# Optimization experiments

Measured on AMD Instinct MI355X. Metric: run time of the kernel, lower is better.

The kernel has to match this reference:

```python
import jax, jax.numpy as jnp
import numpy as np

NUM_HEADS = 16


def setup_inputs() -> dict:
    key = jax.random.key(0)
    ks = jax.random.split(key, 4)
    B, S, D = 2, 2048, 1024
    scale = 1.0 / np.sqrt(D)
    x = jax.random.normal(ks[0], (B, S, D), dtype=jnp.float32)
    Wq = jax.random.normal(ks[1], (D, D), dtype=jnp.float32) * scale
    Wk = jax.random.normal(ks[2], (D, D), dtype=jnp.float32) * scale
    Wv = jax.random.normal(ks[3], (D, D), dtype=jnp.float32) * scale
    bq = jnp.zeros((D,), dtype=jnp.float32)
    bk = jnp.zeros((D,), dtype=jnp.float32)
    bv = jnp.zeros((D,), dtype=jnp.float32)
    return {"x": x, "Wq": Wq, "bq": bq, "Wk": Wk, "bk": bk, "Wv": Wv, "bv": bv}


def _split_heads(t, H):
    B, S, D = t.shape
    return t.reshape(B, S, H, D // H).transpose(0, 2, 1, 3)  # (B,H,S,depth)


def reference(x, Wq, bq, Wk, bk, Wv, bv):
    H = NUM_HEADS
    B, S, D = x.shape
    depth = D // H
    q = _split_heads(x @ Wq + bq, H)
    k = _split_heads(x @ Wk + bk, H)
    v = _split_heads(x @ Wv + bv, H)
    # causal mask: strictly-upper-triangular ones, added as finfo.min * mask
    mask = 1.0 - jnp.tril(jnp.ones((S, S), dtype=jnp.float32))
    scores = jnp.einsum("bhqd,bhkd->bhqk", q, k) / jnp.sqrt(jnp.float32(depth))
    scores = scores + jnp.float32(np.finfo(np.float32).min) * mask
    probs = jax.nn.softmax(scores, axis=-1)
    att = jnp.einsum("bhqk,bhkd->bhqd", probs, v)
    return att.transpose(0, 2, 1, 3).reshape(B, S, D)
```

## Files before the change

### kernel.cpp

```cpp
#include <hip/hip_runtime.h>
#include <hip/hip_bf16.h>

#define B_ 2
#define S_ 2048
#define D_ 1024
#define H_ 16
#define DH 64
#define M_ (B_*S_)
#define NT_ (S_/64)

using bf16x8 = __attribute__((ext_vector_type(8))) __bf16;
using f32x4  = __attribute__((ext_vector_type(4))) float;

__device__ __forceinline__ int swz(int row) { return ((row ^ (row >> 3)) & 7) << 3; }

__device__ __forceinline__ void glds16(const __bf16* g, __bf16* l) {
#if __has_builtin(__builtin_amdgcn_global_load_lds)
  __builtin_amdgcn_global_load_lds(
      (const __attribute__((address_space(1))) unsigned int*)g,
      (__attribute__((address_space(3))) unsigned int*)l, 16, 0, 0);
#else
  *(bf16x8*)l = *(const bf16x8*)g;
#endif
}

__global__ __launch_bounds__(256) void conv_x(const float* __restrict__ x,
                                              __bf16* __restrict__ xb) {
  int idx = blockIdx.x * 256 + threadIdx.x;
  int m = idx >> 7, k = (idx & 127) * 8;
  float4 a = *(const float4*)&x[(size_t)m * D_ + k];
  float4 b = *(const float4*)&x[(size_t)m * D_ + k + 4];
  bf16x8 o;
  o[0]=(__bf16)a.x; o[1]=(__bf16)a.y; o[2]=(__bf16)a.z; o[3]=(__bf16)a.w;
  o[4]=(__bf16)b.x; o[5]=(__bf16)b.y; o[6]=(__bf16)b.z; o[7]=(__bf16)b.w;
  *(bf16x8*)&xb[(size_t)m * D_ + (k & ~63) + ((k & 63) ^ swz(m))] = o;
}

__global__ __launch_bounds__(256) void conv_w(const float* __restrict__ Wq,
                                              const float* __restrict__ Wk,
                                              const float* __restrict__ Wv,
                                              __bf16* __restrict__ wt) {
  int z = blockIdx.z;
  const float* __restrict__ W = (z == 0) ? Wq : (z == 1) ? Wk : Wv;
  __bf16* __restrict__ Wt = wt + (size_t)z * D_ * D_;
  __shared__ __bf16 Lt[64 * 66];
  int tid = threadIdx.x;
  int k0 = blockIdx.x * 64, n0 = blockIdx.y * 64;
  #pragma unroll
  for (int i = 0; i < 4; ++i) {
    int f4 = i * 256 + tid;
    int r = f4 >> 4, c4 = (f4 & 15) * 4;
    float4 v = *(const float4*)&W[(size_t)(k0 + r) * D_ + n0 + c4];
    Lt[(c4 + 0) * 66 + r] = (__bf16)v.x;
    Lt[(c4 + 1) * 66 + r] = (__bf16)v.y;
    Lt[(c4 + 2) * 66 + r] = (__bf16)v.z;
    Lt[(c4 + 3) * 66 + r] = (__bf16)v.w;
  }
  __syncthreads();
  #pragma unroll
  for (int i = 0; i < 2; ++i) {
    int idx = i * 256 + tid;
    int n = idx >> 3, kc = (idx & 7) * 8;
    int nf = n0 + n;
    bf16x8 o;
    #pragma unroll
    for (int j = 0; j < 8; ++j) o[j] = Lt[n * 66 + kc + j];
    *(bf16x8*)&Wt[(size_t)nf * D_ + k0 + (kc ^ swz(nf))] = o;
  }
}

#define BM 256
#define BN 256
#define BK 64
#define NKT (D_/BK)

__global__ __launch_bounds__(512) void qkv_gemm(
    const __bf16* __restrict__ xb, const __bf16* __restrict__ wt,
    const float* __restrict__ bq, const float* __restrict__ bk,
    const float* __restrict__ bv, __bf16* __restrict__ qkv) {
  int z = blockIdx.z;
  const __bf16* __restrict__ Wt = wt + (size_t)z * D_ * D_;
  const float* __restrict__ bias = (z == 0) ? bq : (z == 1) ? bk : bv;
  __bf16* __restrict__ out = qkv + (size_t)z * M_ * D_;
  const float scale = (z == 0) ? 0.125f : 1.0f;

  __shared__ __bf16 Al[2][BM * BK];
  __shared__ __bf16 Bl[2][BM * BK];

  int tid = threadIdx.x, lane = tid & 63, w = tid >> 6;
  int m0 = blockIdx.y * BM, n0 = blockIdx.x * BN;
  int wr = (w >> 2) * 128;
  int wc = (w & 3) * 64;

  f32x4 acc[8][4] = {};

#define STAGE(buf, kt)                                                        \
  {                                                                           \
    int k0 = (kt) * BK;                                                       \
    _Pragma("unroll")                                                         \
    for (int r = 0; r < 4; ++r) {                                             \
      int e = (r * 512 + tid) * 8;                                            \
      int row = e >> 6, col = e & 63;                                         \
      glds16(&xb[(size_t)(m0 + row) * D_ + k0 + col], &Al[buf][e]);           \
      glds16(&Wt[(size_t)(n0 + row) * D_ + k0 + col], &Bl[buf][e]);           \
    }                                                                         \
  }

  STAGE(0, 0);
  __syncthreads();

  int cur = 0;
  for (int kt = 0; kt < NKT; ++kt) {
    if (kt + 1 < NKT) STAGE(cur ^ 1, kt + 1);
    #pragma unroll
    for (int kk = 0; kk < 2; ++kk) {
      bf16x8 af[8], bfr[4];
      #pragma unroll
      for (int mi = 0; mi < 8; ++mi) {
        int row = wr + mi * 16 + (lane & 15);
        af[mi] = *(const bf16x8*)&Al[cur][row * 64 +
                 ((kk * 32 + (lane >> 4) * 8) ^ swz(row))];
      }
      #pragma unroll
      for (int ni = 0; ni < 4; ++ni) {
        int col = wc + ni * 16 + (lane & 15);
        bfr[ni] = *(const bf16x8*)&Bl[cur][col * 64 +
                  ((kk * 32 + (lane >> 4) * 8) ^ swz(col))];
      }
      #pragma unroll
      for (int mi = 0; mi < 8; ++mi)
        #pragma unroll
        for (int ni = 0; ni < 4; ++ni)
          acc[mi][ni] = __builtin_amdgcn_mfma_f32_16x16x32_bf16(
              af[mi], bfr[ni], acc[mi][ni], 0, 0, 0);
    }
    __syncthreads();
    cur ^= 1;
  }
#undef STAGE

  #pragma unroll
  for (int mi = 0; mi < 8; ++mi) {
    #pragma unroll
    for (int ni = 0; ni < 4; ++ni) {
      int col = n0 + wc + ni * 16 + (lane & 15);
      int h = col >> 6, dh = col & 63;
      float bv_ = bias[col];
      #pragma unroll
      for (int r = 0; r < 4; ++r) {
        int row = m0 + wr + mi * 16 + (lane >> 4) * 4 + r;
        int b = row >> 11, s = row & 2047;
        out[((size_t)(b * H_ + h) * S_ + s) * DH + dh] =
            (__bf16)((acc[mi][ni][r] + bv_) * scale);
      }
    }
  }
}

__global__ __launch_bounds__(256) void vtrans(const __bf16* __restrict__ v,
                                              __bf16* __restrict__ vt) {
  __shared__ __bf16 Lt[64 * 64];
  int tid = threadIdx.x;
  int s0 = blockIdx.x * 64;
  int h = blockIdx.y, b = blockIdx.z;
  const __bf16* __restrict__ src = v + ((size_t)(b * H_ + h)) * S_ * DH;
  __bf16* __restrict__ dst = vt + ((size_t)(b * H_ + h)) * DH * S_;
  #pragma unroll
  for (int i = 0; i < 2; ++i) {
    int e = (i * 256 + tid) * 8;
    int s = e >> 6, d0 = e & 63;
    bf16x8 r = *(const bf16x8*)&src[(size_t)(s0 + s) * DH + d0];
    #pragma unroll
    for (int j = 0; j < 8; ++j) {
      int d = d0 + j;
      Lt[d * 64 + (s ^ swz(d))] = r[j];
    }
  }
  __syncthreads();
  #pragma unroll
  for (int i = 0; i < 2; ++i) {
    int e = (i * 256 + tid) * 8;
    int d = e >> 6, sc = e & 63;
    bf16x8 o = *(const bf16x8*)&Lt[d * 64 + (sc ^ swz(d))];
    *(bf16x8*)&dst[(size_t)d * S_ + s0 + sc] = o;
  }
}

__device__ __forceinline__ void attn_tile_sw(
    const bf16x8* aq, f32x4* accO, float& m_reg, float& l_reg,
    const __bf16* __restrict__ Kl, const __bf16* __restrict__ Vt,
    __bf16* __restrict__ Plw, int lane, int kv0, int qbase, bool diag) {
  const int g = lane >> 4;
  const int ql = lane & 15;
  f32x4 sfT[4];
  __builtin_amdgcn_s_setprio(1);
  #pragma unroll
  for (int f = 0; f < 4; ++f) {
    f32x4 zz = {};
    int row = f * 16 + ql;
    int sr = swz(row);
    #pragma unroll
    for (int kk = 0; kk < 2; ++kk) {
      bf16x8 ka = *(const bf16x8*)&Kl[row * 64 + ((kk * 32 + g * 8) ^ sr)];
      zz = __builtin_amdgcn_mfma_f32_16x16x32_bf16(ka, aq[kk], zz, 0, 0, 0);
    }
    sfT[f] = zz;
  }
  __builtin_amdgcn_s_setprio(0);

  if (diag) {
    int qg = qbase + ql;
    #pragma unroll
    for (int f = 0; f < 4; ++f)
      #pragma unroll
      for (int r = 0; r < 4; ++r)
        if (kv0 + f * 16 + g * 4 + r > qg) sfT[f][r] = -1e30f;
  }

  float mx = sfT[0][0];
  #pragma unroll
  for (int f = 0; f < 4; ++f)
    #pragma unroll
    for (int r = 0; r < 4; ++r) mx = fmaxf(mx, sfT[f][r]);
  mx = fmaxf(mx, __shfl_xor(mx, 16, 64));
  mx = fmaxf(mx, __shfl_xor(mx, 32, 64));
  float mnew = fmaxf(m_reg, mx);
  float alpha = __expf(m_reg - mnew);
  m_reg = mnew;
  float rs = 0.f;
  #pragma unroll
  for (int f = 0; f < 4; ++f)
    #pragma unroll
    for (int r = 0; r < 4; ++r) {
      float p = __expf(sfT[f][r] - mnew);
      sfT[f][r] = p;
      rs += p;
    }
  rs += __shfl_xor(rs, 16, 64);
  rs += __shfl_xor(rs, 32, 64);
  l_reg = l_reg * alpha + rs;

  const int key = (ql & 7) << 3;
  #pragma unroll
  for (int f = 0; f < 4; ++f)
    #pragma unroll
    for (int r = 0; r < 4; ++r)
      Plw[ql * 64 + ((f * 16 + g * 4 + r) ^ key)] = (__bf16)sfT[f][r];

  float ab[4];
  #pragma unroll
  for (int r = 0; r < 4; ++r) ab[r] = __shfl(alpha, g * 4 + r, 16);
  #pragma unroll
  for (int f = 0; f < 4; ++f)
    #pragma unroll
    for (int r = 0; r < 4; ++r) accO[f][r] *= ab[r];

  __builtin_amdgcn_s_setprio(1);
  #pragma unroll
  for (int kk = 0; kk < 2; ++kk) {
    bf16x8 pa = *(const bf16x8*)&Plw[ql * 64 + ((kk * 32 + g * 8) ^ key)];
    #pragma unroll
    for (int f = 0; f < 4; ++f) {
      int vrow = f * 16 + ql;
      bf16x8 vb = *(const bf16x8*)&Vt[vrow * 64 + ((kk * 32 + g * 8) ^ swz(vrow))];
      accO[f] = __builtin_amdgcn_mfma_f32_16x16x32_bf16(pa, vb, accO[f], 0, 0, 0);
    }
  }
  __builtin_amdgcn_s_setprio(0);
}

__device__ __forceinline__ void attn_out_sw(
    const f32x4* accO, float l_reg, float* __restrict__ out,
    int b, int h, int qbase, int lane) {
  float lr[4];
  #pragma unroll
  for (int r = 0; r < 4; ++r) lr[r] = __shfl(l_reg, (lane >> 4) * 4 + r, 16);
  #pragma unroll
  for (int f = 0; f < 4; ++f) {
    int dh = f * 16 + (lane & 15);
    #pragma unroll
    for (int r = 0; r < 4; ++r) {
      int qg = qbase + (lane >> 4) * 4 + r;
      out[((size_t)(b * S_ + qg)) * D_ + h * DH + dh] = accO[f][r] / lr[r];
    }
  }
}

__global__ __launch_bounds__(256) void attn(
    const __bf16* __restrict__ Q, const __bf16* __restrict__ K,
    const __bf16* __restrict__ VT, float* __restrict__ out) {
  __shared__ __bf16 Kl[64 * 64];
  __shared__ __bf16 Vt[64 * 64];
  __shared__ __bf16 Pl[4][16 * 64];

  int tid = threadIdx.x, lane = tid & 63, w = tid >> 6;
  int bx = blockIdx.x, h = blockIdx.y, b = blockIdx.z;
  int qA0 = bx * 64, qB0 = (NT_ - 1 - bx) * 64;
  size_t base = ((size_t)(b * H_ + h)) * S_ * DH;
  const __bf16* __restrict__ Qg = Q + base;
  const __bf16* __restrict__ Kg = K + base;
  const __bf16* __restrict__ VTg = VT + base;

  bf16x8 aqA[2], aqB[2];
  int qra = qA0 + w * 16 + (lane & 15), qrb = qB0 + w * 16 + (lane & 15);
  #pragma unroll
  for (int kk = 0; kk < 2; ++kk) {
    aqA[kk] = *(const bf16x8*)&Qg[(size_t)qra * DH + kk * 32 + (lane >> 4) * 8];
    aqB[kk] = *(const bf16x8*)&Qg[(size_t)qrb * DH + kk * 32 + (lane >> 4) * 8];
  }

  f32x4 accA[4] = {}, accB[4] = {};
  float mA = -1e30f, lA = 0.f, mB = -1e30f, lB = 0.f;

  const int ktA = bx, ktB = NT_ - 1 - bx;

  bf16x8 kreg[2], vreg[2];
  #pragma unroll
  for (int i = 0; i < 2; ++i) {
    int e = (i * 256 + tid) * 8;
    kreg[i] = *(const bf16x8*)&Kg[(size_t)(e >> 6) * DH + (e & 63)];
    vreg[i] = *(const bf16x8*)&VTg[(size_t)(e >> 6) * S_ + (e & 63)];
  }

  for (int kt = 0; kt <= ktB; ++kt) {
    int kv0 = kt * 64;
    #pragma unroll
    for (int i = 0; i < 2; ++i) {
      int e = (i * 256 + tid) * 8;
      int rrow = e >> 6, cc = e & 63;
      *(bf16x8*)&Kl[rrow * 64 + (cc ^ swz(rrow))] = kreg[i];
      *(bf16x8*)&Vt[rrow * 64 + (cc ^ swz(rrow))] = vreg[i];
    }
    __syncthreads();

    if (kt < ktB) {
      int kvn = kv0 + 64;
      #pragma unroll
      for (int i = 0; i < 2; ++i) {
        int e = (i * 256 + tid) * 8;
        kreg[i] = *(const bf16x8*)&Kg[(size_t)(kvn + (e >> 6)) * DH + (e & 63)];
        vreg[i] = *(const bf16x8*)&VTg[(size_t)(e >> 6) * S_ + kvn + (e & 63)];
      }
    }

    attn_tile_sw(aqB, accB, mB, lB, Kl, Vt, Pl[w], lane, kv0, qB0 + w * 16,
                 kt == ktB);
    if (kt <= ktA)
      attn_tile_sw(aqA, accA, mA, lA, Kl, Vt, Pl[w], lane, kv0, qA0 + w * 16,
                   kt == ktA);
    __syncthreads();
  }

  attn_out_sw(accA, lA, out, b, h, qA0 + w * 16, lane);
  attn_out_sw(accB, lB, out, b, h, qB0 + w * 16, lane);
}

extern "C" void kernel_launch(void* const* d_in, const int* in_sizes, int n_in,
                              void* d_out, int out_size, void* d_ws, size_t ws_size,
                              hipStream_t stream) {
  const float* x  = (const float*)d_in[0];
  const float* Wq = (const float*)d_in[1];
  const float* bq = (const float*)d_in[2];
  const float* Wk = (const float*)d_in[3];
  const float* bk = (const float*)d_in[4];
  const float* Wv = (const float*)d_in[5];
  const float* bv = (const float*)d_in[6];
  float* out = (float*)d_out;

  __bf16* xb  = (__bf16*)d_ws;
  __bf16* wt  = xb + (size_t)M_ * D_;
  __bf16* qkv = wt + (size_t)3 * D_ * D_;
  __bf16* wsq = qkv;
  __bf16* wsk = qkv + (size_t)M_ * D_;
  __bf16* wsv = qkv + (size_t)2 * M_ * D_;
  __bf16* vtg = xb;

  conv_x<<<(M_ * (D_ / 8)) / 256, 256, 0, stream>>>(x, xb);
  conv_w<<<dim3(D_ / 64, D_ / 64, 3), 256, 0, stream>>>(Wq, Wk, Wv, wt);
  qkv_gemm<<<dim3(D_ / BN, M_ / BM, 3), 512, 0, stream>>>(xb, wt, bq, bk, bv, qkv);
  vtrans<<<dim3(S_ / 64, H_, B_), 256, 0, stream>>>(wsv, vtg);
  attn<<<dim3(NT_ / 2, H_, B_), 256, 0, stream>>>(wsq, wsk, vtg, out);
}
```

Measured before the change: 189.6 us.

## Shrink QKV GEMM tiles and streamline softmax with exp2, lazy rescale, packed bf16

The QKV GEMM moves from 256x256 tiles with 512 threads to 128x128 tiles with 256 threads. That raises the block count from 192 to 768, which should fill the CUs better at some cost in data reuse. The attention softmax folds log2(e) into the Q scale so it can use exp2f, and it skips rescaling the accumulator and running sum unless the max rises past a threshold, for which it relies on a warp-wide vote. P is converted to bf16 two values at a time with v_cvt_pk_bf16_f32 in inline asm, and the max reduction is restructured as a tree.

```diff
diff --git a/kernel.cpp b/kernel.cpp
--- a/kernel.cpp
+++ b/kernel.cpp
@@ -69,12 +69,10 @@
   }
 }
 
-#define BM 256
-#define BN 256
 #define BK 64
 #define NKT (D_/BK)
 
-__global__ __launch_bounds__(512) void qkv_gemm(
+__global__ __launch_bounds__(256) void qkv_gemm(
     const __bf16* __restrict__ xb, const __bf16* __restrict__ wt,
     const float* __restrict__ bq, const float* __restrict__ bk,
     const float* __restrict__ bv, __bf16* __restrict__ qkv) {
@@ -82,24 +80,23 @@
   const __bf16* __restrict__ Wt = wt + (size_t)z * D_ * D_;
   const float* __restrict__ bias = (z == 0) ? bq : (z == 1) ? bk : bv;
   __bf16* __restrict__ out = qkv + (size_t)z * M_ * D_;
-  const float scale = (z == 0) ? 0.125f : 1.0f;
-
-  __shared__ __bf16 Al[2][BM * BK];
-  __shared__ __bf16 Bl[2][BM * BK];
+  const float scale = (z == 0) ? 0.18033688f : 1.0f;
+
+  __shared__ __bf16 Al[2][128 * 64];
+  __shared__ __bf16 Bl[2][128 * 64];
 
   int tid = threadIdx.x, lane = tid & 63, w = tid >> 6;
-  int m0 = blockIdx.y * BM, n0 = blockIdx.x * BN;
-  int wr = (w >> 2) * 128;
-  int wc = (w & 3) * 64;
-
-  f32x4 acc[8][4] = {};
+  int m0 = blockIdx.y * 128, n0 = blockIdx.x * 128;
+  int wr = (w >> 1) * 64, wc = (w & 1) * 64;
+
+  f32x4 acc[4][4] = {};
 
 #define STAGE(buf, kt)                                                        \
   {                                                                           \
     int k0 = (kt) * BK;                                                       \
     _Pragma("unroll")                                                         \
     for (int r = 0; r < 4; ++r) {                                             \
-      int e = (r * 512 + tid) * 8;                                            \
+      int e = (r * 256 + tid) * 8;                                            \
       int row = e >> 6, col = e & 63;                                         \
       glds16(&xb[(size_t)(m0 + row) * D_ + k0 + col], &Al[buf][e]);           \
       glds16(&Wt[(size_t)(n0 + row) * D_ + k0 + col], &Bl[buf][e]);           \
@@ -114,9 +111,9 @@
     if (kt + 1 < NKT) STAGE(cur ^ 1, kt + 1);
     #pragma unroll
     for (int kk = 0; kk < 2; ++kk) {
-      bf16x8 af[8], bfr[4];
-      #pragma unroll
-      for (int mi = 0; mi < 8; ++mi) {
+      bf16x8 af[4], bfr[4];
+      #pragma unroll
+      for (int mi = 0; mi < 4; ++mi) {
         int row = wr + mi * 16 + (lane & 15);
         af[mi] = *(const bf16x8*)&Al[cur][row * 64 +
                  ((kk * 32 + (lane >> 4) * 8) ^ swz(row))];
@@ -128,7 +125,7 @@
                   ((kk * 32 + (lane >> 4) * 8) ^ swz(col))];
       }
       #pragma unroll
-      for (int mi = 0; mi < 8; ++mi)
+      for (int mi = 0; mi < 4; ++mi)
         #pragma unroll
         for (int ni = 0; ni < 4; ++ni)
           acc[mi][ni] = __builtin_amdgcn_mfma_f32_16x16x32_bf16(
@@ -140,7 +137,7 @@
 #undef STAGE
 
   #pragma unroll
-  for (int mi = 0; mi < 8; ++mi) {
+  for (int mi = 0; mi < 4; ++mi) {
     #pragma unroll
     for (int ni = 0; ni < 4; ++ni) {
       int col = n0 + wc + ni * 16 + (lane & 15);
@@ -217,43 +214,51 @@
         if (kv0 + f * 16 + g * 4 + r > qg) sfT[f][r] = -1e30f;
   }
 
-  float mx = sfT[0][0];
-  #pragma unroll
-  for (int f = 0; f < 4; ++f)
-    #pragma unroll
-    for (int r = 0; r < 4; ++r) mx = fmaxf(mx, sfT[f][r]);
+  float mx = fmaxf(fmaxf(sfT[0][0], sfT[0][1]), fmaxf(sfT[0][2], sfT[0][3]));
+  #pragma unroll
+  for (int f = 1; f < 4; ++f)
+    mx = fmaxf(mx, fmaxf(fmaxf(sfT[f][0], sfT[f][1]),
+                         fmaxf(sfT[f][2], sfT[f][3])));
   mx = fmaxf(mx, __shfl_xor(mx, 16, 64));
   mx = fmaxf(mx, __shfl_xor(mx, 32, 64));
-  float mnew = fmaxf(m_reg, mx);
-  float alpha = __expf(m_reg - mnew);
-  m_reg = mnew;
+
+  if (!__all(mx <= m_reg + 11.54f)) {
+    float mnew = fmaxf(m_reg, mx);
+    float alpha = exp2f(m_reg - mnew);
+    m_reg = mnew;
+    float ab[4];
+    #pragma unroll
+    for (int r = 0; r < 4; ++r) ab[r] = __shfl(alpha, g * 4 + r, 16);
+    #pragma unroll
+    for (int f = 0; f < 4; ++f)
+      #pragma unroll
+      for (int r = 0; r < 4; ++r) accO[f][r] *= ab[r];
+    l_reg *= alpha;
+  }
+
   float rs = 0.f;
   #pragma unroll
   for (int f = 0; f < 4; ++f)
     #pragma unroll
     for (int r = 0; r < 4; ++r) {
-      float p = __expf(sfT[f][r] - mnew);
+      float p = exp2f(sfT[f][r] - m_reg);
       sfT[f][r] = p;
       rs += p;
     }
   rs += __shfl_xor(rs, 16, 64);
   rs += __shfl_xor(rs, 32, 64);
-  l_reg = l_reg * alpha + rs;
+  l_reg += rs;
 
   const int key = (ql & 7) << 3;
   #pragma unroll
   for (int f = 0; f < 4; ++f)
     #pragma unroll
-    for (int r = 0; r < 4; ++r)
-      Plw[ql * 64 + ((f * 16 + g * 4 + r) ^ key)] = (__bf16)sfT[f][r];
-
-  float ab[4];
-  #pragma unroll
-  for (int r = 0; r < 4; ++r) ab[r] = __shfl(alpha, g * 4 + r, 16);
-  #pragma unroll
-  for (int f = 0; f < 4; ++f)
-    #pragma unroll
-    for (int r = 0; r < 4; ++r) accO[f][r] *= ab[r];
+    for (int rp = 0; rp < 2; ++rp) {
+      unsigned u;
+      asm volatile("v_cvt_pk_bf16_f32 %0, %1, %2"
+                   : "=v"(u) : "v"(sfT[f][2 * rp]), "v"(sfT[f][2 * rp + 1]));
+      *(unsigned*)&Plw[ql * 64 + ((f * 16 + g * 4 + 2 * rp) ^ key)] = u;
+    }
 
   __builtin_amdgcn_s_setprio(1);
   #pragma unroll
@@ -377,7 +382,7 @@
 
   conv_x<<<(M_ * (D_ / 8)) / 256, 256, 0, stream>>>(x, xb);
   conv_w<<<dim3(D_ / 64, D_ / 64, 3), 256, 0, stream>>>(Wq, Wk, Wv, wt);
-  qkv_gemm<<<dim3(D_ / BN, M_ / BM, 3), 512, 0, stream>>>(xb, wt, bq, bk, bv, qkv);
+  qkv_gemm<<<dim3(D_ / 128, M_ / 128, 3), 256, 0, stream>>>(xb, wt, bq, bk, bv, qkv);
   vtrans<<<dim3(S_ / 64, H_, B_), 256, 0, stream>>>(wsv, vtg);
   attn<<<dim3(NT_ / 2, H_, B_), 256, 0, stream>>>(wsq, wsk, vtg, out);
 }
```

Result: slower. 195.8 us (+3.3%).
